# Performance work log

Measured on AMD Instinct MI355X. Metric: run time of the kernel, lower is better.

The kernel has to match this reference:

```python
import jax, jax.numpy as jnp
import numpy as np
from jax import lax

IN_FEATURES = 1024
NUM_TAGS = 128
C = NUM_TAGS + 3          # CRF adds start/stop (+1 pad slot per original code)
START_IDX = C - 2
STOP_IDX = C - 1
NEG = -10000.0


def setup_inputs() -> dict:
    key = jax.random.key(0)
    k1, k2, k3, k4 = jax.random.split(key, 4)
    B, L = 64, 512
    x = jax.random.normal(k1, (B, L, IN_FEATURES), dtype=jnp.float32)
    mask = jnp.ones((B, L), dtype=jnp.float32)
    W = jax.random.normal(k2, (C, IN_FEATURES), dtype=jnp.float32) * (1.0 / np.sqrt(IN_FEATURES))
    b = jax.random.normal(k3, (C,), dtype=jnp.float32) * 0.01
    transitions = jax.random.normal(k4, (C, C), dtype=jnp.float32)
    # transitions[i, j] = score of transitioning FROM j TO i
    transitions = transitions.at[START_IDX, :].set(NEG)   # never transition into start
    transitions = transitions.at[:, STOP_IDX].set(NEG)    # never transition out of stop
    return {"x": x, "mask": mask, "W": W, "b": b, "transitions": transitions}


def reference(x, mask, W, b, transitions):
    """CRF forward: linear projection + Viterbi decode.
    Returns (best_score [B], best_paths [B, L])."""
    feats = jnp.einsum("bld,cd->blc", x, W) + b          # [B, L, C]
    B, L, Cn = feats.shape

    init_score = jnp.full((B, Cn), NEG, dtype=feats.dtype).at[:, START_IDX].set(0.0)

    def viterbi_step(score, inp):
        feat_t, mask_t = inp                              # [B, C], [B]
        # acc[b, i, j] = score[b, j] + transitions[i, j]
        acc = score[:, None, :] + transitions[None, :, :]  # [B, C, C]
        best = jnp.max(acc, axis=-1)                      # [B, C]
        bp = jnp.argmax(acc, axis=-1).astype(jnp.int32)   # [B, C]
        m = mask_t[:, None]
        new_score = (best + feat_t) * m + score * (1.0 - m)
        return new_score, bp

    final_score, bps = lax.scan(
        viterbi_step, init_score,
        (jnp.transpose(feats, (1, 0, 2)), mask.T))        # bps: [L, B, C]

    final_score = final_score + transitions[STOP_IDX]     # [B, C]
    best_score = jnp.max(final_score, axis=-1)            # [B]
    best_tag = jnp.argmax(final_score, axis=-1).astype(jnp.int32)  # [B]

    def backtrack(tag, bp_t):
        # tag: current tag at timestep t; bp_t: [B, C] backpointers at t
        prev = jnp.take_along_axis(bp_t, tag[:, None], axis=1)[:, 0]
        return prev, tag                                  # emit tag at timestep t

    _, path = lax.scan(backtrack, best_tag, bps, reverse=True)  # path: [L, B]
    best_paths = path.T                                   # [B, L]
    return best_score, best_paths
```

## Files before the change

### kernel.cpp

```cpp
#include <hip/hip_runtime.h>

#define BB 64
#define LL 512
#define DD 1024
#define CC 131
#define CP 132
#define START_I 129
#define STOP_I 130
#define NEGV -10000.0f

__device__ __forceinline__ void lds_barrier() {
    asm volatile("s_waitcnt lgkmcnt(0)" ::: "memory");
    __builtin_amdgcn_s_barrier();
    __builtin_amdgcn_sched_barrier(0);
}

#define RL(src, i) __int_as_float(__builtin_amdgcn_readlane(__float_as_int(src), (i)))

#define GM 64
#define GK 32
#define LSTR 36

__global__ __launch_bounds__(256, 2) void gemm_feats(
    const float* __restrict__ x, const float* __restrict__ W,
    const float* __restrict__ bias, float* __restrict__ feats)
{
    __shared__ float xs[GM * LSTR];
    __shared__ float ws[CP * LSTR];

    const int tid = threadIdx.x;
    const int m0 = blockIdx.x * GM;
    const int tm = tid & 15;
    const int tj = (tid >> 4) & 15;
    const bool tail = (tj < 3);
    const int tjt = (tj < 3) ? tj : 2;

    float acc[4][8];
    float acct[4];
#pragma unroll
    for (int r = 0; r < 4; ++r) {
        acct[r] = 0.f;
#pragma unroll
        for (int c = 0; c < 8; ++c) acc[r][c] = 0.f;
    }

    for (int kc = 0; kc < DD / GK; ++kc) {
        const int k0 = kc * GK;
        if (kc) __syncthreads();
#pragma unroll
        for (int q = 0; q < 2; ++q) {
            int lin = tid + q * 256;
            int m = lin >> 3, c4 = lin & 7;
            float4 v = *(const float4*)&x[(size_t)(m0 + m) * DD + k0 + c4 * 4];
            *(float4*)&xs[m * LSTR + c4 * 4] = v;
        }
#pragma unroll
        for (int q = 0; q < 5; ++q) {
            int lin = tid + q * 256;
            if (lin < CC * 8) {
                int r = lin >> 3, c4 = lin & 7;
                float4 v = *(const float4*)&W[(size_t)r * DD + k0 + c4 * 4];
                *(float4*)&ws[r * LSTR + c4 * 4] = v;
            }
        }
        __syncthreads();

#pragma unroll
        for (int k4 = 0; k4 < 8; ++k4) {
            float4 xr[4], wr[8], wt;
#pragma unroll
            for (int r = 0; r < 4; ++r)
                xr[r] = *(const float4*)&xs[(tm + 16 * r) * LSTR + k4 * 4];
#pragma unroll
            for (int c = 0; c < 8; ++c)
                wr[c] = *(const float4*)&ws[(tj + 16 * c) * LSTR + k4 * 4];
            wt = *(const float4*)&ws[(128 + tjt) * LSTR + k4 * 4];
#pragma unroll
            for (int r = 0; r < 4; ++r) {
#pragma unroll
                for (int c = 0; c < 8; ++c) {
                    acc[r][c] = fmaf(xr[r].x, wr[c].x, acc[r][c]);
                    acc[r][c] = fmaf(xr[r].y, wr[c].y, acc[r][c]);
                    acc[r][c] = fmaf(xr[r].z, wr[c].z, acc[r][c]);
                    acc[r][c] = fmaf(xr[r].w, wr[c].w, acc[r][c]);
                }
                acct[r] = fmaf(xr[r].x, wt.x, acct[r]);
                acct[r] = fmaf(xr[r].y, wt.y, acct[r]);
                acct[r] = fmaf(xr[r].z, wt.z, acct[r]);
                acct[r] = fmaf(xr[r].w, wt.w, acct[r]);
            }
        }
    }

#pragma unroll
    for (int c = 0; c < 8; ++c) {
        int j = tj + 16 * c;
        float bv = bias[j];
#pragma unroll
        for (int r = 0; r < 4; ++r)
            feats[(size_t)(m0 + tm + 16 * r) * CP + j] = acc[r][c] + bv;
    }
    if (tail) {
        int j = 128 + tj;
        float bv = bias[j];
#pragma unroll
        for (int r = 0; r < 4; ++r)
            feats[(size_t)(m0 + tm + 16 * r) * CP + j] = acct[r] + bv;
    }
}

__global__ __launch_bounds__(192, 1) void viterbi_fwd(
    const float* __restrict__ feats, const float* __restrict__ mask,
    const float* __restrict__ trans, float* __restrict__ hist)
{
    const int b = blockIdx.x;
    const int tid = threadIdx.x;
    const int wave = tid >> 6, lane = tid & 63;
    const int colc = (wave < 2) ? (wave * 64 + lane)
                                : (128 + ((lane < 2) ? lane : 2));
    const bool owner = (wave < 2) || (lane < 3);

    __shared__ float sbuf[2][132];

    float4 T[33];
    {
        const float* tr = trans + (size_t)colc * CC;
#pragma unroll
        for (int q = 0; q < 32; ++q) {
            T[q].x = tr[4 * q + 0]; T[q].y = tr[4 * q + 1];
            T[q].z = tr[4 * q + 2]; T[q].w = tr[4 * q + 3];
        }
        T[32].x = tr[128]; T[32].y = tr[129]; T[32].z = tr[130];
        T[32].w = NEGV;
    }
#pragma unroll
    for (int q = 0; q < 33; ++q)
        asm volatile("" : "+v"(T[q].x), "+v"(T[q].y), "+v"(T[q].z), "+v"(T[q].w));

    for (int q = tid; q < 2 * 132; q += 192) {
        int bufi = q / 132, idx = q - bufi * 132;
        sbuf[bufi][idx] = (bufi == 0 && idx == START_I) ? 0.f : NEGV;
    }
    __syncthreads();

    const float* fb = feats + (size_t)b * LL * CP;
    const float* mb = mask + (size_t)b * LL;
    float* hb = hist + (size_t)b * LL * CP;

    float s_reg = (colc == START_I) ? 0.f : NEGV;

    float fv0 = fb[colc], fv1 = fb[CP + colc];
    float mv0 = mb[0], mv1 = mb[1];
    const float* fb_t = fb + 2 * CP + colc;
    const float* mb_t = mb + 2;
    float* hb_t = hb + colc;

    int cur = 0;
    float ns_p = 0.f;

    for (int t = 0; t < LL; ++t) {
        if (t > 0) {
            if (owner) *hb_t = ns_p;
            hb_t += CP;
        }
        float fv2 = 0.f, mv2 = 1.f;
        if (t + 2 < LL) { fv2 = *fb_t; mv2 = *mb_t; }
        fb_t += CP; ++mb_t;

        float sa = sbuf[cur][lane];
        float sb = sbuf[cur][64 + lane];
        float s128 = sbuf[cur][128], s129 = sbuf[cur][129], s130 = sbuf[cur][130];

        float a0 = -3.0e38f, a1 = -3.0e38f, a2 = -3.0e38f, a3 = -3.0e38f;
#pragma unroll
        for (int q = 0; q < 16; ++q) {
            float4 t4 = T[q];
            a0 = fmaxf(fmaxf(RL(sa, 4 * q + 0) + t4.x, RL(sa, 4 * q + 1) + t4.y), a0);
            a1 = fmaxf(fmaxf(RL(sa, 4 * q + 2) + t4.z, RL(sa, 4 * q + 3) + t4.w), a1);
        }
#pragma unroll
        for (int q = 0; q < 16; ++q) {
            float4 t4 = T[16 + q];
            a2 = fmaxf(fmaxf(RL(sb, 4 * q + 0) + t4.x, RL(sb, 4 * q + 1) + t4.y), a2);
            a3 = fmaxf(fmaxf(RL(sb, 4 * q + 2) + t4.z, RL(sb, 4 * q + 3) + t4.w), a3);
        }
        {
            float4 t4 = T[32];
            a0 = fmaxf(fmaxf(s128 + t4.x, s129 + t4.y), a0);
            a1 = fmaxf(a1, s130 + t4.z);
        }
        float best = fmaxf(fmaxf(a0, a1), fmaxf(a2, a3));

        float ns = (mv0 != 0.f) ? (best + fv0) : s_reg;
        s_reg = ns;
        if (owner) sbuf[cur ^ 1][colc] = ns;
        ns_p = ns;

        lds_barrier();

        fv0 = fv1; fv1 = fv2; mv0 = mv1; mv1 = mv2;
        cur ^= 1;
    }
    if (owner) *hb_t = ns_p;
}

__global__ __launch_bounds__(256, 4) void bp_kernel(
    const float* __restrict__ hist, const float* __restrict__ trans,
    unsigned char* __restrict__ bp)
{
    const int b  = blockIdx.x / 5;
    const int jc = blockIdx.x % 5;
    const int tc = blockIdx.y;
    const int tid = threadIdx.x;
    const int j0 = jc * 32;

    __shared__ float Ts[32][136];
    __shared__ float hs[8][132];

    for (int q = 0; q < 17; ++q) {
        int lin = tid + q * 256;
        if (lin < 32 * CC) {
            int r = lin / CC, i = lin - r * CC;
            if (j0 + r < CC) Ts[r][i] = trans[(size_t)(j0 + r) * CC + i];
        }
    }
    {
        const float4* src = (const float4*)(hist + ((size_t)b * LL + tc * 8) * CP);
#pragma unroll
        for (int q = 0; q < 2; ++q) {
            int lin = tid + q * 256;
            if (lin < (8 * CP) / 4) ((float4*)hs)[lin] = src[lin];
        }
    }
    __syncthreads();

    const int jl = tid & 31;
    const int tt = tid >> 5;
    const int j = j0 + jl;
    const int t = tc * 8 + tt + 1;
    if (j >= CC || t >= LL) return;

    float best; int idx;
    {
        float4 tv = *(const float4*)&Ts[jl][128];
        float4 hv = *(const float4*)&hs[tt][128];
        best = hv.z + tv.z; idx = 130;
        float v;
        v = hv.y + tv.y; if (v >= best) { best = v; idx = 129; }
        v = hv.x + tv.x; if (v >= best) { best = v; idx = 128; }
    }
#pragma unroll
    for (int i4 = 31; i4 >= 0; --i4) {
        float4 tv = *(const float4*)&Ts[jl][i4 * 4];
        float4 hv = *(const float4*)&hs[tt][i4 * 4];
        float v;
        v = hv.w + tv.w; if (v >= best) { best = v; idx = i4 * 4 + 3; }
        v = hv.z + tv.z; if (v >= best) { best = v; idx = i4 * 4 + 2; }
        v = hv.y + tv.y; if (v >= best) { best = v; idx = i4 * 4 + 1; }
        v = hv.x + tv.x; if (v >= best) { best = v; idx = i4 * 4 + 0; }
    }
    bp[((size_t)b * LL + t) * CP + j] = (unsigned char)idx;
}

__global__ __launch_bounds__(64, 1) void viterbi_btr(
    const float* __restrict__ hist, const float* __restrict__ trans,
    const unsigned char* __restrict__ bp,
    float* __restrict__ out_score, float* __restrict__ out_path)
{
    const int b = blockIdx.x;
    const int lane = threadIdx.x;
    const float* hb = hist + ((size_t)b * LL + (LL - 1)) * CP;
    const float* ts = trans + (size_t)STOP_I * CC;

    float v0 = hb[lane] + ts[lane];
    float v1 = hb[lane + 64] + ts[lane + 64];
    float v2 = (lane < 3) ? (hb[lane + 128] + ts[lane + 128]) : -3.0e38f;

    float best = v0; int idx = lane;
    if (v1 > best) { best = v1; idx = lane + 64; }
    if (v2 > best) { best = v2; idx = lane + 128; }
#pragma unroll
    for (int off = 32; off >= 1; off >>= 1) {
        float ob = __shfl_xor(best, off, 64);
        int   oi = __shfl_xor(idx, off, 64);
        if (ob > best || (ob == best && oi < idx)) { best = ob; idx = oi; }
    }

    float* op = out_path + (size_t)b * LL;
    if (lane == 0) {
        out_score[b] = best;
        op[LL - 1] = (float)idx;
    }
    int tag = idx;

    __shared__ unsigned char buf[2][1088];
    const unsigned char* bpb = bp + (size_t)b * LL * CP;

    {
        const unsigned int* src = (const unsigned int*)(bpb + (size_t)504 * CP);
        unsigned int* dst = (unsigned int*)buf[1];
#pragma unroll
        for (int q = 0; q < 5; ++q) {
            int lin = lane + q * 64;
            if (lin < 264) dst[lin] = src[lin];
        }
    }
    lds_barrier();

    int cur = 1;
    for (int k = 63; k >= 0; --k) {
        unsigned int r0 = 0, r1 = 0, r2 = 0, r3 = 0, r4 = 0;
        if (k > 0) {
            const unsigned int* src = (const unsigned int*)(bpb + (size_t)(k - 1) * 8 * CP);
            r0 = src[lane];
            r1 = src[lane + 64];
            r2 = src[lane + 128];
            r3 = src[lane + 192];
            if (lane < 8) r4 = src[lane + 256];
        }
        const unsigned char* cb = buf[cur];
#pragma unroll
        for (int s = 7; s >= 0; --s) {
            int t = k * 8 + s;
            if (t >= 1) {
                tag = cb[s * CP + tag];
                if (lane == 0) op[t - 1] = (float)tag;
            }
        }
        if (k > 0) {
            unsigned int* dst = (unsigned int*)buf[cur ^ 1];
            dst[lane] = r0;
            dst[lane + 64] = r1;
            dst[lane + 128] = r2;
            dst[lane + 192] = r3;
            if (lane < 8) dst[lane + 256] = r4;
            lds_barrier();
        }
        cur ^= 1;
    }
}

extern "C" void kernel_launch(void* const* d_in, const int* in_sizes, int n_in,
                              void* d_out, int out_size, void* d_ws, size_t ws_size,
                              hipStream_t stream)
{
    const float* x     = (const float*)d_in[0];
    const float* mask  = (const float*)d_in[1];
    const float* W     = (const float*)d_in[2];
    const float* bias  = (const float*)d_in[3];
    const float* trans = (const float*)d_in[4];

    float* feats = (float*)d_ws;
    float* hist  = feats + (size_t)BB * LL * CP;
    unsigned char* bp = (unsigned char*)(hist + (size_t)BB * LL * CP);
    float* out_score = (float*)d_out;
    float* out_path  = out_score + BB;

    hipLaunchKernelGGL(gemm_feats, dim3((BB * LL) / GM), dim3(256), 0, stream, x, W, bias, feats);
    hipLaunchKernelGGL(viterbi_fwd, dim3(BB), dim3(192), 0, stream, feats, mask, trans, hist);
    hipLaunchKernelGGL(bp_kernel, dim3(BB * 5, 64), dim3(256), 0, stream, hist, trans, bp);
    hipLaunchKernelGGL(viterbi_btr, dim3(BB), dim3(64), 0, stream, hist, trans, bp, out_score, out_path);
}
```

Baseline: 732.6 us.

## Split Viterbi max-reduction across four sub-waves per row with LDS partials

```diff
diff --git a/kernel.cpp b/kernel.cpp
--- a/kernel.cpp
+++ b/kernel.cpp
@@ -14,8 +14,6 @@
     __builtin_amdgcn_s_barrier();
     __builtin_amdgcn_sched_barrier(0);
 }
-
-#define RL(src, i) __int_as_float(__builtin_amdgcn_readlane(__float_as_int(src), (i)))
 
 #define GM 64
 #define GK 32
@@ -109,37 +107,49 @@
     }
 }
 
-__global__ __launch_bounds__(192, 1) void viterbi_fwd(
+__global__ __launch_bounds__(576, 1) void viterbi_fwd(
     const float* __restrict__ feats, const float* __restrict__ mask,
     const float* __restrict__ trans, float* __restrict__ hist)
 {
     const int b = blockIdx.x;
     const int tid = threadIdx.x;
-    const int wave = tid >> 6, lane = tid & 63;
-    const int colc = (wave < 2) ? (wave * 64 + lane)
-                                : (128 + ((lane < 2) ? lane : 2));
-    const bool owner = (wave < 2) || (lane < 3);
-
-    __shared__ float sbuf[2][132];
-
-    float4 T[33];
+    const int w = tid >> 6, lane = tid & 63;
+
+    int row, sub;
+    bool scw;
+    if (w < 8) {
+        row = (w >> 2) * 64 + lane;
+        sub = w & 3;
+        scw = true;
+    } else {
+        int r = 128 + (lane >> 2);
+        row = (r <= 130) ? r : 130;
+        sub = lane & 3;
+        scw = (lane < 12);
+    }
+
+    __shared__ float sbuf[2][160];
+    __shared__ float pbuf[4][136];
+
+    float4 T[10];
     {
-        const float* tr = trans + (size_t)colc * CC;
-#pragma unroll
-        for (int q = 0; q < 32; ++q) {
-            T[q].x = tr[4 * q + 0]; T[q].y = tr[4 * q + 1];
-            T[q].z = tr[4 * q + 2]; T[q].w = tr[4 * q + 3];
-        }
-        T[32].x = tr[128]; T[32].y = tr[129]; T[32].z = tr[130];
-        T[32].w = NEGV;
-    }
-#pragma unroll
-    for (int q = 0; q < 33; ++q)
-        asm volatile("" : "+v"(T[q].x), "+v"(T[q].y), "+v"(T[q].z), "+v"(T[q].w));
-
-    for (int q = tid; q < 2 * 132; q += 192) {
-        int bufi = q / 132, idx = q - bufi * 132;
-        sbuf[bufi][idx] = (bufi == 0 && idx == START_I) ? 0.f : NEGV;
+        const float* tr = trans + (size_t)row * CC;
+        const int base = sub * 40;
+#pragma unroll
+        for (int q = 0; q < 10; ++q) {
+            float vx = NEGV, vy = NEGV, vz = NEGV, vw = NEGV;
+            int i = base + 4 * q;
+            if (i + 0 < CC) vx = tr[i + 0];
+            if (i + 1 < CC) vy = tr[i + 1];
+            if (i + 2 < CC) vz = tr[i + 2];
+            if (i + 3 < CC) vw = tr[i + 3];
+            T[q].x = vx; T[q].y = vy; T[q].z = vz; T[q].w = vw;
+        }
+    }
+
+    for (int q = tid; q < 2 * 160; q += 576) {
+        int bi = q / 160, idx = q - bi * 160;
+        sbuf[bi][idx] = (bi == 0 && idx == START_I) ? 0.f : NEGV;
     }
     __syncthreads();
 
@@ -147,61 +157,56 @@
     const float* mb = mask + (size_t)b * LL;
     float* hb = hist + (size_t)b * LL * CP;
 
-    float s_reg = (colc == START_I) ? 0.f : NEGV;
-
-    float fv0 = fb[colc], fv1 = fb[CP + colc];
-    float mv0 = mb[0], mv1 = mb[1];
-    const float* fb_t = fb + 2 * CP + colc;
+    const int k = tid;
+    const bool cmb = (tid < 131);
+    float s_prev = (k == START_I) ? 0.f : NEGV;
+    float fv0 = 0.f, fv1 = 0.f, mv0 = 1.f, mv1 = 1.f;
+    const float* fb_t = fb + 2 * CP + k;
     const float* mb_t = mb + 2;
-    float* hb_t = hb + colc;
-
-    int cur = 0;
-    float ns_p = 0.f;
+    float* hb_k = hb + k;
+    if (cmb) { fv0 = fb[k]; fv1 = fb[CP + k]; mv0 = mb[0]; mv1 = mb[1]; }
 
     for (int t = 0; t < LL; ++t) {
-        if (t > 0) {
-            if (owner) *hb_t = ns_p;
-            hb_t += CP;
-        }
-        float fv2 = 0.f, mv2 = 1.f;
-        if (t + 2 < LL) { fv2 = *fb_t; mv2 = *mb_t; }
-        fb_t += CP; ++mb_t;
-
-        float sa = sbuf[cur][lane];
-        float sb = sbuf[cur][64 + lane];
-        float s128 = sbuf[cur][128], s129 = sbuf[cur][129], s130 = sbuf[cur][130];
-
-        float a0 = -3.0e38f, a1 = -3.0e38f, a2 = -3.0e38f, a3 = -3.0e38f;
-#pragma unroll
-        for (int q = 0; q < 16; ++q) {
-            float4 t4 = T[q];
-            a0 = fmaxf(fmaxf(RL(sa, 4 * q + 0) + t4.x, RL(sa, 4 * q + 1) + t4.y), a0);
-            a1 = fmaxf(fmaxf(RL(sa, 4 * q + 2) + t4.z, RL(sa, 4 * q + 3) + t4.w), a1);
-        }
-#pragma unroll
-        for (int q = 0; q < 16; ++q) {
-            float4 t4 = T[16 + q];
-            a2 = fmaxf(fmaxf(RL(sb, 4 * q + 0) + t4.x, RL(sb, 4 * q + 1) + t4.y), a2);
-            a3 = fmaxf(fmaxf(RL(sb, 4 * q + 2) + t4.z, RL(sb, 4 * q + 3) + t4.w), a3);
-        }
+        const int rb = t & 1;
+
         {
-            float4 t4 = T[32];
-            a0 = fmaxf(fmaxf(s128 + t4.x, s129 + t4.y), a0);
-            a1 = fmaxf(a1, s130 + t4.z);
-        }
-        float best = fmaxf(fmaxf(a0, a1), fmaxf(a2, a3));
-
-        float ns = (mv0 != 0.f) ? (best + fv0) : s_reg;
-        s_reg = ns;
-        if (owner) sbuf[cur ^ 1][colc] = ns;
-        ns_p = ns;
+            const float4* s4 = (const float4*)sbuf[rb] + sub * 10;
+            float a0 = -3.0e38f, a1 = -3.0e38f, a2 = -3.0e38f, a3 = -3.0e38f;
+#pragma unroll
+            for (int q = 0; q < 5; ++q) {
+                float4 sv = s4[q]; float4 t4 = T[q];
+                a0 = fmaxf(fmaxf(sv.x + t4.x, sv.y + t4.y), a0);
+                a1 = fmaxf(fmaxf(sv.z + t4.z, sv.w + t4.w), a1);
+            }
+#pragma unroll
+            for (int q = 5; q < 10; ++q) {
+                float4 sv = s4[q]; float4 t4 = T[q];
+                a2 = fmaxf(fmaxf(sv.x + t4.x, sv.y + t4.y), a2);
+                a3 = fmaxf(fmaxf(sv.z + t4.z, sv.w + t4.w), a3);
+            }
+            if (scw) pbuf[sub][row] = fmaxf(fmaxf(a0, a1), fmaxf(a2, a3));
+        }
 
         lds_barrier();
 
-        fv0 = fv1; fv1 = fv2; mv0 = mv1; mv1 = mv2;
-        cur ^= 1;
-    }
-    if (owner) *hb_t = ns_p;
+        if (cmb) {
+            float fv2 = 0.f, mv2 = 1.f;
+            if (t + 2 < LL) { fv2 = *fb_t; mv2 = *mb_t; }
+            fb_t += CP; ++mb_t;
+
+            float p = fmaxf(fmaxf(pbuf[0][k], pbuf[1][k]),
+                            fmaxf(pbuf[2][k], pbuf[3][k]));
+            float ns = (mv0 != 0.f) ? (p + fv0) : s_prev;
+            s_prev = ns;
+            sbuf[rb ^ 1][k] = ns;
+            *hb_k = ns;
+            hb_k += CP;
+
+            fv0 = fv1; fv1 = fv2; mv0 = mv1; mv1 = mv2;
+        }
+
+        lds_barrier();
+    }
 }
 
 __global__ __launch_bounds__(256, 4) void bp_kernel(
@@ -357,7 +362,7 @@
     float* out_path  = out_score + BB;
 
     hipLaunchKernelGGL(gemm_feats, dim3((BB * LL) / GM), dim3(256), 0, stream, x, W, bias, feats);
-    hipLaunchKernelGGL(viterbi_fwd, dim3(BB), dim3(192), 0, stream, feats, mask, trans, hist);
+    hipLaunchKernelGGL(viterbi_fwd, dim3(BB), dim3(576), 0, stream, feats, mask, trans, hist);
     hipLaunchKernelGGL(bp_kernel, dim3(BB * 5, 64), dim3(256), 0, stream, hist, trans, bp);
     hipLaunchKernelGGL(viterbi_btr, dim3(BB), dim3(64), 0, stream, hist, trans, bp, out_score, out_path);
 }
```

After: 682.3 us. -6.9%, faster.

## Split Viterbi forward max-reduction across 8 waves with partial maxima in LDS

Applied to the files above, without the earlier changes.

```diff
diff --git a/kernel.cpp b/kernel.cpp
--- a/kernel.cpp
+++ b/kernel.cpp
@@ -109,99 +109,104 @@
     }
 }
 
-__global__ __launch_bounds__(192, 1) void viterbi_fwd(
+__global__ __launch_bounds__(512, 1) void viterbi_fwd(
     const float* __restrict__ feats, const float* __restrict__ mask,
     const float* __restrict__ trans, float* __restrict__ hist)
 {
     const int b = blockIdx.x;
     const int tid = threadIdx.x;
-    const int wave = tid >> 6, lane = tid & 63;
-    const int colc = (wave < 2) ? (wave * 64 + lane)
-                                : (128 + ((lane < 2) ? lane : 2));
-    const bool owner = (wave < 2) || (lane < 3);
-
-    __shared__ float sbuf[2][132];
-
-    float4 T[33];
+    const int w = tid >> 6, lane = tid & 63;
+    const int jg = w >> 2;
+    const int sub = w & 3;
+    const int j = jg * 64 + lane;
+    const int i0 = sub * 33;
+    const int ic = i0 + lane;
+    const bool cl = (lane < 33) && (ic < CC);
+    const bool hw = (jg == 0) && cl;
+
+    __shared__ float pbuf[2][4][136];
+
+    float Tk[33];
     {
-        const float* tr = trans + (size_t)colc * CC;
-#pragma unroll
-        for (int q = 0; q < 32; ++q) {
-            T[q].x = tr[4 * q + 0]; T[q].y = tr[4 * q + 1];
-            T[q].z = tr[4 * q + 2]; T[q].w = tr[4 * q + 3];
-        }
-        T[32].x = tr[128]; T[32].y = tr[129]; T[32].z = tr[130];
-        T[32].w = NEGV;
-    }
-#pragma unroll
-    for (int q = 0; q < 33; ++q)
-        asm volatile("" : "+v"(T[q].x), "+v"(T[q].y), "+v"(T[q].z), "+v"(T[q].w));
-
-    for (int q = tid; q < 2 * 132; q += 192) {
-        int bufi = q / 132, idx = q - bufi * 132;
-        sbuf[bufi][idx] = (bufi == 0 && idx == START_I) ? 0.f : NEGV;
-    }
-    __syncthreads();
+        const float* tr = trans + (size_t)j * CC + i0;
+#pragma unroll
+        for (int k = 0; k < 33; ++k)
+            Tk[k] = (i0 + k < CC) ? tr[k] : NEGV;
+    }
+    float tA = NEGV, tB = NEGV, tC = NEGV;
+    if (jg == 0 && cl) {
+        tA = trans[(size_t)128 * CC + ic];
+        tB = trans[(size_t)129 * CC + ic];
+        tC = trans[(size_t)130 * CC + ic];
+    }
 
     const float* fb = feats + (size_t)b * LL * CP;
     const float* mb = mask + (size_t)b * LL;
     float* hb = hist + (size_t)b * LL * CP;
 
-    float s_reg = (colc == START_I) ? 0.f : NEGV;
-
-    float fv0 = fb[colc], fv1 = fb[CP + colc];
+    float sa = (cl && ic == START_I) ? 0.f : NEGV;
+
+#define SCAN(WB)                                                                  \
+    {                                                                             \
+        float a0 = -3.0e38f, a1 = -3.0e38f;                                       \
+        _Pragma("unroll")                                                         \
+        for (int q = 0; q < 8; ++q) {                                             \
+            a0 = fmaxf(fmaxf(RL(sa, 4*q+0) + Tk[4*q+0],                           \
+                             RL(sa, 4*q+1) + Tk[4*q+1]), a0);                     \
+            a1 = fmaxf(fmaxf(RL(sa, 4*q+2) + Tk[4*q+2],                           \
+                             RL(sa, 4*q+3) + Tk[4*q+3]), a1);                     \
+        }                                                                         \
+        a0 = fmaxf(a0, RL(sa, 32) + Tk[32]);                                      \
+        pbuf[WB][sub][j] = fmaxf(a0, a1);                                         \
+        if (jg == 0) {                                                            \
+            float cA = cl ? (sa + tA) : -3.0e38f;                                 \
+            float cB = cl ? (sa + tB) : -3.0e38f;                                 \
+            float cC = cl ? (sa + tC) : -3.0e38f;                                 \
+            _Pragma("unroll")                                                     \
+            for (int off = 1; off < 64; off <<= 1) {                              \
+                cA = fmaxf(cA, __shfl_xor(cA, off, 64));                          \
+                cB = fmaxf(cB, __shfl_xor(cB, off, 64));                          \
+                cC = fmaxf(cC, __shfl_xor(cC, off, 64));                          \
+            }                                                                     \
+            if (lane == 0) {                                                      \
+                pbuf[WB][sub][128] = cA;                                          \
+                pbuf[WB][sub][129] = cB;                                          \
+                pbuf[WB][sub][130] = cC;                                          \
+            }                                                                     \
+        }                                                                         \
+    }
+
+    SCAN(0)
+    lds_barrier();
+
+    float fv0 = 0.f, fv1 = 0.f;
+    if (cl) { fv0 = fb[ic]; fv1 = fb[CP + ic]; }
     float mv0 = mb[0], mv1 = mb[1];
-    const float* fb_t = fb + 2 * CP + colc;
+    const float* fb_t = fb + 2 * CP + ic;
     const float* mb_t = mb + 2;
-    float* hb_t = hb + colc;
-
-    int cur = 0;
-    float ns_p = 0.f;
+    float* hb_t = hb + ic;
 
     for (int t = 0; t < LL; ++t) {
-        if (t > 0) {
-            if (owner) *hb_t = ns_p;
-            hb_t += CP;
-        }
+        const int rb = t & 1, wb = rb ^ 1;
         float fv2 = 0.f, mv2 = 1.f;
-        if (t + 2 < LL) { fv2 = *fb_t; mv2 = *mb_t; }
+        if (t + 2 < LL) { if (cl) fv2 = *fb_t; mv2 = *mb_t; }
         fb_t += CP; ++mb_t;
 
-        float sa = sbuf[cur][lane];
-        float sb = sbuf[cur][64 + lane];
-        float s128 = sbuf[cur][128], s129 = sbuf[cur][129], s130 = sbuf[cur][130];
-
-        float a0 = -3.0e38f, a1 = -3.0e38f, a2 = -3.0e38f, a3 = -3.0e38f;
-#pragma unroll
-        for (int q = 0; q < 16; ++q) {
-            float4 t4 = T[q];
-            a0 = fmaxf(fmaxf(RL(sa, 4 * q + 0) + t4.x, RL(sa, 4 * q + 1) + t4.y), a0);
-            a1 = fmaxf(fmaxf(RL(sa, 4 * q + 2) + t4.z, RL(sa, 4 * q + 3) + t4.w), a1);
-        }
-#pragma unroll
-        for (int q = 0; q < 16; ++q) {
-            float4 t4 = T[16 + q];
-            a2 = fmaxf(fmaxf(RL(sb, 4 * q + 0) + t4.x, RL(sb, 4 * q + 1) + t4.y), a2);
-            a3 = fmaxf(fmaxf(RL(sb, 4 * q + 2) + t4.z, RL(sb, 4 * q + 3) + t4.w), a3);
-        }
-        {
-            float4 t4 = T[32];
-            a0 = fmaxf(fmaxf(s128 + t4.x, s129 + t4.y), a0);
-            a1 = fmaxf(a1, s130 + t4.z);
-        }
-        float best = fmaxf(fmaxf(a0, a1), fmaxf(a2, a3));
-
-        float ns = (mv0 != 0.f) ? (best + fv0) : s_reg;
-        s_reg = ns;
-        if (owner) sbuf[cur ^ 1][colc] = ns;
-        ns_p = ns;
+        if (cl) {
+            float p01 = fmaxf(pbuf[rb][0][ic], pbuf[rb][1][ic]);
+            float p23 = fmaxf(pbuf[rb][2][ic], pbuf[rb][3][ic]);
+            float ns = (mv0 != 0.f) ? (fmaxf(p01, p23) + fv0) : sa;
+            sa = ns;
+            if (hw) *hb_t = ns;
+        }
+        hb_t += CP;
+
+        if (t < LL - 1) SCAN(wb)
 
         lds_barrier();
-
         fv0 = fv1; fv1 = fv2; mv0 = mv1; mv1 = mv2;
-        cur ^= 1;
-    }
-    if (owner) *hb_t = ns_p;
+    }
+#undef SCAN
 }
 
 __global__ __launch_bounds__(256, 4) void bp_kernel(
@@ -357,7 +362,7 @@
     float* out_path  = out_score + BB;
 
     hipLaunchKernelGGL(gemm_feats, dim3((BB * LL) / GM), dim3(256), 0, stream, x, W, bias, feats);
-    hipLaunchKernelGGL(viterbi_fwd, dim3(BB), dim3(192), 0, stream, feats, mask, trans, hist);
+    hipLaunchKernelGGL(viterbi_fwd, dim3(BB), dim3(512), 0, stream, feats, mask, trans, hist);
     hipLaunchKernelGGL(bp_kernel, dim3(BB * 5, 64), dim3(256), 0, stream, hist, trans, bp);
     hipLaunchKernelGGL(viterbi_btr, dim3(BB), dim3(64), 0, stream, hist, trans, bp, out_score, out_path);
 }
```

Measured after the change: 737.7 us. No clear change (+0.7%).
